# Performance work log

Hardware: AMD Instinct MI355X
Metric: run time of the kernel (lower is better)

## Reference

```python
import jax, jax.numpy as jnp
import numpy as np

HIDDEN = 4096
NH = 32        # num attention heads
NKV = 8        # num key/value heads
HD = 128       # q/k head dim
VHD = 96       # v head dim
ROT = 64       # rotary dim = int(HD * 0.5)
THETA = 10000.0
B, S = 2, 2048


def setup_inputs() -> dict:
    key = jax.random.key(0)
    ks = jax.random.split(key, 6)
    w = 0.02
    return {
        "hidden_states": jax.random.normal(ks[0], (B, S, HIDDEN), jnp.float32),
        "position_ids": jnp.arange(B * S, dtype=jnp.int32).reshape(B, S) % S,
        "Wq": jax.random.normal(ks[1], (NH * HD, HIDDEN), jnp.float32) * w,
        "Wk": jax.random.normal(ks[2], (NKV * HD, HIDDEN), jnp.float32) * w,
        "Wv": jax.random.normal(ks[3], (NKV * VHD, HIDDEN), jnp.float32) * w,
        "Wo": jax.random.normal(ks[4], (HIDDEN, NH * VHD), jnp.float32) * w,
    }


def _rotate_half(x):
    x1, x2 = x[..., : x.shape[-1] // 2], x[..., x.shape[-1] // 2 :]
    return jnp.concatenate((-x2, x1), axis=-1)


def reference(hidden_states, position_ids, Wq, Wk, Wv, Wo):
    b, s, _ = hidden_states.shape
    # QKV projections (torch Linear: y = x @ W^T)
    q = (hidden_states @ Wq.T).reshape(b, s, NH, HD).transpose(0, 2, 1, 3)   # [b,NH,s,HD]
    k = (hidden_states @ Wk.T).reshape(b, s, NKV, HD).transpose(0, 2, 1, 3)  # [b,NKV,s,HD]
    v = (hidden_states @ Wv.T).reshape(b, s, NKV, VHD).transpose(0, 2, 1, 3)  # [b,NKV,s,VHD]

    # rotary embedding over first ROT dims (partial RoPE)
    inv_freq = 1.0 / (THETA ** (jnp.arange(0, ROT, 2, dtype=jnp.float32) / ROT))  # [ROT/2]
    freqs = position_ids.astype(jnp.float32)[:, :, None] * inv_freq              # [b,s,ROT/2]
    emb = jnp.concatenate((freqs, freqs), axis=-1)                                # [b,s,ROT]
    cos = jnp.cos(emb)[:, None, :, :].astype(hidden_states.dtype)                 # [b,1,s,ROT]
    sin = jnp.sin(emb)[:, None, :, :].astype(hidden_states.dtype)

    q_rot, q_pass = q[..., :ROT], q[..., ROT:]
    k_rot, k_pass = k[..., :ROT], k[..., ROT:]
    q_rot = q_rot * cos + _rotate_half(q_rot) * sin
    k_rot = k_rot * cos + _rotate_half(k_rot) * sin
    q = jnp.concatenate((q_rot, q_pass), axis=-1)
    k = jnp.concatenate((k_rot, k_pass), axis=-1)

    # GQA: repeat_kv (repeat_interleave over head dim)
    n_rep = NH // NKV
    k = jnp.repeat(k, n_rep, axis=1)  # [b,NH,s,HD]
    v = jnp.repeat(v, n_rep, axis=1)  # [b,NH,s,VHD]

    scores = jnp.einsum("bhqd,bhkd->bhqk", q, k) / np.float32(np.sqrt(HD))
    # causal additive mask (attention_mask as built by the HF model)
    neg = jnp.finfo(jnp.float32).min
    causal = jnp.where(jnp.tril(jnp.ones((s, s), dtype=bool)), 0.0, neg)
    scores = scores + causal[None, None, :, :]

    attn = jax.nn.softmax(scores.astype(jnp.float32), axis=-1).astype(q.dtype)
    out = jnp.einsum("bhqk,bhkd->bhqd", attn, v)          # [b,NH,s,VHD]
    out = out.transpose(0, 2, 1, 3).reshape(b, s, NH * VHD)
    return out @ Wo.T                                      # [b,s,HIDDEN]
```

## Files before the change

kernel.cpp:

```cpp
#include <hip/hip_runtime.h>

typedef __attribute__((ext_vector_type(4))) float f32x4;
typedef __attribute__((ext_vector_type(8))) __bf16 bf16x8;
typedef __attribute__((ext_vector_type(8))) unsigned short u16x8;
typedef __attribute__((ext_vector_type(4))) unsigned short u16x4;
typedef __attribute__((ext_vector_type(4))) short s16x4;
typedef unsigned short ushort_t;

__device__ __forceinline__ unsigned short f2bf(float x) {
  unsigned u = __builtin_bit_cast(unsigned, x);
  u += 0x7fffu + ((u >> 16) & 1u);
  return (unsigned short)(u >> 16);
}
__device__ __forceinline__ float bf2f(unsigned short h) {
  unsigned u = ((unsigned)h) << 16;
  return __builtin_bit_cast(float, u);
}
__device__ __forceinline__ short f2bf_n(float x) {
  return __builtin_bit_cast(short, (__bf16)x);
}

__device__ __forceinline__ void gload_lds16(const void* g, void* l) {
  __builtin_amdgcn_global_load_lds(
      (const __attribute__((address_space(1))) unsigned int*)g,
      (__attribute__((address_space(3))) unsigned int*)l, 16, 0, 0);
}

__global__ __launch_bounds__(256) void k_f32_to_bf16(
    const float* __restrict__ src, ushort_t* __restrict__ dst, int n8) {
  int i = blockIdx.x * 256 + threadIdx.x;
  if (i >= n8) return;
  float4 a = ((const float4*)src)[i * 2 + 0];
  float4 b = ((const float4*)src)[i * 2 + 1];
  u16x8 o;
  o[0] = f2bf(a.x); o[1] = f2bf(a.y); o[2] = f2bf(a.z); o[3] = f2bf(a.w);
  o[4] = f2bf(b.x); o[5] = f2bf(b.y); o[6] = f2bf(b.z); o[7] = f2bf(b.w);
  ((u16x8*)dst)[i] = o;
}

template <int OUT_BF16, int ROPE>
__global__ __launch_bounds__(256, 4) void k_gemm_bt(
    const ushort_t* __restrict__ A, const ushort_t* __restrict__ B,
    void* __restrict__ C, int K, int lda, int ldb, int ldc,
    const int* __restrict__ pos_ids) {
  __shared__ ushort_t lA[128 * 64];
  __shared__ ushort_t lB[128 * 64];
  const int t = threadIdx.x;
  const int ln = t & 63, w = t >> 6;
  const int fr = ln & 15, fg = ln >> 4;
  const int m0 = blockIdx.x * 128, n0 = blockIdx.y * 128;
  const int wr = (w >> 1) * 64, wc = (w & 1) * 64;

  const int srow = t >> 3;
  const int scol = ((((t & 7) * 16) ^ ((srow & 7) << 4)) >> 1);
  const ushort_t* pA = A + (srow + m0) * lda + scol;
  const ushort_t* pB = B + (srow + n0) * ldb + scol;
  char* lAb = (char*)lA + (w << 10);
  char* lBb = (char*)lB + (w << 10);

  f32x4 acc[4][4] = {};

  for (int k0 = 0; k0 < K; k0 += 64) {
    __syncthreads();
#pragma unroll
    for (int i = 0; i < 4; ++i) {
      gload_lds16(pA + i * 32 * lda + k0, lAb + i * 4096);
      gload_lds16(pB + i * 32 * ldb + k0, lBb + i * 4096);
    }
    __syncthreads();
#pragma unroll
    for (int kh = 0; kh < 2; ++kh) {
      bf16x8 af[4], bfv[4];
#pragma unroll
      for (int m = 0; m < 4; ++m) {
        int row = wr + m * 16 + fr;
        af[m] = *(const bf16x8*)((const char*)lA + row * 128 +
                                 ((kh * 64 + fg * 16) ^ ((row & 7) << 4)));
      }
#pragma unroll
      for (int n = 0; n < 4; ++n) {
        int row = wc + n * 16 + fr;
        bfv[n] = *(const bf16x8*)((const char*)lB + row * 128 +
                                  ((kh * 64 + fg * 16) ^ ((row & 7) << 4)));
      }
#pragma unroll
      for (int m = 0; m < 4; ++m)
#pragma unroll
        for (int n = 0; n < 4; ++n)
          acc[m][n] = __builtin_amdgcn_mfma_f32_16x16x32_bf16(
              af[m], bfv[n], acc[m][n], 0, 0, 0);
    }
  }

  if (ROPE) {
    if (n0 < 5120 && wc == 0) {
#pragma unroll
      for (int n = 0; n < 2; ++n) {
        const float fi = (float)(n * 16 + fr);
        const float inv = exp2f(-fi * (13.287712379549449f / 32.0f));
#pragma unroll
        for (int m = 0; m < 4; ++m) {
          const int row = m0 + wr + m * 16 + fg * 4;
#pragma unroll
          for (int j = 0; j < 4; ++j) {
            const float ang = (float)pos_ids[row + j] * inv;
            float sn, cs;
            __sincosf(ang, &sn, &cs);
            const float x1 = acc[m][n][j], x2 = acc[m][n + 2][j];
            acc[m][n][j]     = x1 * cs - x2 * sn;
            acc[m][n + 2][j] = x2 * cs + x1 * sn;
          }
        }
      }
    }
  }

#pragma unroll
  for (int m = 0; m < 4; ++m)
#pragma unroll
    for (int n = 0; n < 4; ++n) {
      int row = m0 + wr + m * 16 + fg * 4;
      int col = n0 + wc + n * 16 + fr;
#pragma unroll
      for (int j = 0; j < 4; ++j) {
        if (OUT_BF16)
          ((ushort_t*)C)[(size_t)(row + j) * ldc + col] = f2bf(acc[m][n][j]);
        else
          ((float*)C)[(size_t)(row + j) * ldc + col] = acc[m][n][j];
      }
    }
}

__global__ __launch_bounds__(512, 2) void k_attn(
    const ushort_t* __restrict__ QKV, ushort_t* __restrict__ O) {
  __shared__ ushort_t lK[64 * 128];
  __shared__ ushort_t lV[16 * 96 * 4];

  const int t = threadIdx.x, ln = t & 63, w = t >> 6;
  const int fr = ln & 15, fg = ln >> 4;
  const int h = blockIdx.y, b = blockIdx.z;
  const int qt = b ? (7 - (int)blockIdx.x) : (int)blockIdx.x;
  const int hk = h >> 2;
  const int q0 = qt * 256 + w * 32;
  const int tb = b * 2048;

  bf16x8 qf[2][4];
#pragma unroll
  for (int rq = 0; rq < 2; ++rq)
#pragma unroll
    for (int kb = 0; kb < 4; ++kb)
      qf[rq][kb] = *(const bf16x8*)(QKV +
                    (size_t)(tb + q0 + rq * 16 + fr) * 5888 + h * 128 +
                    kb * 32 + fg * 8);

  f32x4 oacc[6][2] = {};
  float mreg[2] = {-1e30f, -1e30f};
  float lreg[2] = {0.f, 0.f};

  const int krow = t >> 4;
  const int kse = ((((t & 15) * 16) ^ (((t >> 4) & 7) << 4)) >> 1);
  const int k4s = t / 12, c8s = t % 12;

  const float sc = 0.088388347648318447f;
  const float l2e = 1.4426950408889634f;
  const float scl2e = sc * l2e;

  u16x8 vrow[4];
  const ushort_t* pVb =
      QKV + (size_t)(tb + k4s * 4) * 5888 + 5120 + hk * 96 + c8s * 8;
  if (t < 192) {
#pragma unroll
    for (int kr = 0; kr < 4; ++kr)
      vrow[kr] = *(const u16x8*)(pVb + (size_t)kr * 5888);
  }

  const int nkt = qt * 4 + 4;
  for (int kt = 0; kt < nkt; ++kt) {
    const int kb0 = kt * 64;
    __syncthreads();
    if (t < 192) {
#pragma unroll
      for (int i = 0; i < 8; ++i) {
        int cs = (c8s * 8 + i) ^ (k4s & 15);
        u16x4 q;
#pragma unroll
        for (int kr = 0; kr < 4; ++kr) q[kr] = vrow[kr][i];
        *(u16x4*)(&lV[(k4s * 96 + cs) * 4]) = q;
      }
    }
    {
      const ushort_t* pK =
          QKV + (size_t)(tb + kb0 + krow) * 5888 + 4096 + hk * 128 + kse;
#pragma unroll
      for (int i = 0; i < 2; ++i)
        gload_lds16(pK + (size_t)i * 32 * 5888,
                    (char*)lK + i * 8192 + (w << 10));
    }
    __builtin_amdgcn_sched_barrier(0);
    const bool pre = (kt + 1 < nkt);
    if (pre && t < 192) {
      const ushort_t* pV = pVb + (size_t)(kb0 + 64) * 5888;
#pragma unroll
      for (int kr = 0; kr < 4; ++kr)
        vrow[kr] = *(const u16x8*)(pV + (size_t)kr * 5888);
    }
    __builtin_amdgcn_sched_barrier(0);
    if (pre && w < 3)
      asm volatile("s_waitcnt vmcnt(4) lgkmcnt(0)" ::: "memory");
    else
      asm volatile("s_waitcnt vmcnt(0) lgkmcnt(0)" ::: "memory");
    __builtin_amdgcn_s_barrier();
    asm volatile("" ::: "memory");
    __builtin_amdgcn_sched_barrier(0);

    if (kb0 > q0 + 31) continue;
    f32x4 s[4][2] = {};
    __builtin_amdgcn_s_setprio(1);
#pragma unroll
    for (int cb = 0; cb < 4; ++cb) {
      const int kv = cb * 16 + fr;
      bf16x8 kf[4];
#pragma unroll
      for (int kb = 0; kb < 4; ++kb)
        kf[kb] = *(const bf16x8*)((const char*)lK + kv * 256 +
                                  ((kb * 64 + fg * 16) ^ ((kv & 7) << 4)));
#pragma unroll
      for (int rq = 0; rq < 2; ++rq)
#pragma unroll
        for (int kb = 0; kb < 4; ++kb)
          s[cb][rq] = __builtin_amdgcn_mfma_f32_16x16x32_bf16(
              kf[kb], qf[rq][kb], s[cb][rq], 0, 0, 0);
    }
    __builtin_amdgcn_s_setprio(0);
    if (kb0 + 63 > q0) {
#pragma unroll
      for (int rq = 0; rq < 2; ++rq) {
        const int qrel = q0 + rq * 16 + fr - kb0;
#pragma unroll
        for (int cb = 0; cb < 4; ++cb)
#pragma unroll
          for (int j = 0; j < 4; ++j)
            if (cb * 16 + fg * 4 + j > qrel) s[cb][rq][j] = -3.0e38f;
      }
    }
    float pmax[2];
#pragma unroll
    for (int rq = 0; rq < 2; ++rq) {
      f32x4 rm4 = s[0][rq];
#pragma unroll
      for (int cb = 1; cb < 4; ++cb)
#pragma unroll
        for (int j = 0; j < 4; ++j) rm4[j] = fmaxf(rm4[j], s[cb][rq][j]);
      float rm = fmaxf(fmaxf(rm4[0], rm4[1]), fmaxf(rm4[2], rm4[3]));
      rm = fmaxf(rm, __shfl_xor(rm, 16, 64));
      rm = fmaxf(rm, __shfl_xor(rm, 32, 64));
      pmax[rq] = rm * sc;
    }
    bool need = (pmax[0] > mreg[0] + 6.f) || (pmax[1] > mreg[1] + 6.f);
    if (__any(need)) {
#pragma unroll
      for (int rq = 0; rq < 2; ++rq) {
        float mnew = fmaxf(mreg[rq], pmax[rq]);
        float sf = exp2f((mreg[rq] - mnew) * l2e);
        mreg[rq] = mnew;
        lreg[rq] *= sf;
#pragma unroll
        for (int c6 = 0; c6 < 6; ++c6) oacc[c6][rq] *= sf;
      }
    }
    s16x4 pb[4][2];
#pragma unroll
    for (int rq = 0; rq < 2; ++rq) {
      const float mb = mreg[rq] * l2e;
      f32x4 ps4 = {};
#pragma unroll
      for (int cb = 0; cb < 4; ++cb) {
#pragma unroll
        for (int j = 0; j < 4; ++j) {
          float p = exp2f(fmaf(s[cb][rq][j], scl2e, -mb));
          s[cb][rq][j] = p;
          ps4[j] += p;
        }
      }
      float ps = (ps4[0] + ps4[1]) + (ps4[2] + ps4[3]);
      ps += __shfl_xor(ps, 16, 64);
      ps += __shfl_xor(ps, 32, 64);
      lreg[rq] += ps;
#pragma unroll
      for (int cb = 0; cb < 4; ++cb) {
        s16x4 v;
#pragma unroll
        for (int j = 0; j < 4; ++j) v[j] = f2bf_n(s[cb][rq][j]);
        pb[cb][rq] = v;
      }
    }
    __builtin_amdgcn_s_setprio(1);
#pragma unroll
    for (int cb = 0; cb < 4; ++cb) {
      const int k4 = cb * 4 + fg;
      s16x4 va[6];
#pragma unroll
      for (int c6 = 0; c6 < 6; ++c6)
        va[c6] = *(const s16x4*)(
            &lV[(k4 * 96 + (((c6 * 16 + fr) ^ (k4 & 15)))) * 4]);
#pragma unroll
      for (int c6 = 0; c6 < 6; ++c6)
#pragma unroll
        for (int rq = 0; rq < 2; ++rq)
          oacc[c6][rq] = __builtin_amdgcn_mfma_f32_16x16x16bf16_1k(
              va[c6], pb[cb][rq], oacc[c6][rq], 0, 0, 0);
    }
    __builtin_amdgcn_s_setprio(0);
  }
#pragma unroll
  for (int rq = 0; rq < 2; ++rq) {
    const float inv = 1.0f / lreg[rq];
    const size_t rowb = (size_t)(tb + q0 + rq * 16 + fr) * 3072 + h * 96;
#pragma unroll
    for (int c6 = 0; c6 < 6; ++c6) {
      u16x4 o;
#pragma unroll
      for (int j = 0; j < 4; ++j)
        o[j] = (unsigned short)f2bf_n(oacc[c6][rq][j] * inv);
      *(u16x4*)(&O[rowb + c6 * 16 + fg * 4]) = o;
    }
  }
}

extern "C" void kernel_launch(void* const* d_in, const int* in_sizes, int n_in,
                              void* d_out, int out_size, void* d_ws,
                              size_t ws_size, hipStream_t stream) {
  const float* X  = (const float*)d_in[0];
  const int*   pos = (const int*)d_in[1];
  const float* Wq = (const float*)d_in[2];
  const float* Wk = (const float*)d_in[3];
  const float* Wv = (const float*)d_in[4];
  const float* Wo = (const float*)d_in[5];
  float* out = (float*)d_out;

  ushort_t* Xb    = (ushort_t*)d_ws;
  ushort_t* Wob   = Xb + 16777216;
  ushort_t* QKV   = Wob + 12582912;
  ushort_t* AO    = QKV + 24117248;
  ushort_t* Wqkvb = (ushort_t*)d_out;

  k_f32_to_bf16<<<8192, 256, 0, stream>>>(X, Xb, 2097152);
  k_f32_to_bf16<<<8192, 256, 0, stream>>>(Wq, Wqkvb, 2097152);
  k_f32_to_bf16<<<2048, 256, 0, stream>>>(Wk, Wqkvb + 16777216, 524288);
  k_f32_to_bf16<<<1536, 256, 0, stream>>>(Wv, Wqkvb + 20971520, 393216);
  k_f32_to_bf16<<<6144, 256, 0, stream>>>(Wo, Wob, 1572864);

  k_gemm_bt<1, 1><<<dim3(32, 46), 256, 0, stream>>>(Xb, Wqkvb, QKV, 4096,
                                                    4096, 4096, 5888, pos);
  k_attn<<<dim3(8, 32, 2), 512, 0, stream>>>(QKV, AO);
  k_gemm_bt<0, 0><<<dim3(32, 32), 256, 0, stream>>>(AO, Wob, out, 3072, 3072,
                                                    3072, 4096, nullptr);
}
```

Before: 477.1 us.

## Double attention KV tile to 128 rows per barrier and fuse weight conversions

The attention kernel now stages 128 K/V rows per loop iteration instead of 64. Each staged tile is processed as two 64-row sub-blocks, so there are half as many block-wide barriers and global-to-LDS load phases per query tile. The cost is more LDS per block (about 56KB) and a coarser causal tail, where part of a staged tile may go unused. Separately, the four weight fp32-to-bf16 conversion launches are merged into one kernel that picks its source by block index, saving launch overhead.

Measured after the change: 455.6 us. 4.5% less time.

```diff
diff --git a/kernel.cpp b/kernel.cpp
--- a/kernel.cpp
+++ b/kernel.cpp
@@ -35,6 +35,27 @@
   u16x8 o;
   o[0] = f2bf(a.x); o[1] = f2bf(a.y); o[2] = f2bf(a.z); o[3] = f2bf(a.w);
   o[4] = f2bf(b.x); o[5] = f2bf(b.y); o[6] = f2bf(b.z); o[7] = f2bf(b.w);
+  ((u16x8*)dst)[i] = o;
+}
+
+__global__ __launch_bounds__(256) void k_w_to_bf16(
+    const float* __restrict__ Wq, const float* __restrict__ Wk,
+    const float* __restrict__ Wv, const float* __restrict__ Wo,
+    ushort_t* __restrict__ dWq, ushort_t* __restrict__ dWk,
+    ushort_t* __restrict__ dWv, ushort_t* __restrict__ dWo) {
+  const int b = blockIdx.x;
+  const float* src;
+  ushort_t* dst;
+  int i;
+  if (b < 8192)       { src = Wq; dst = dWq; i = b * 256 + threadIdx.x; }
+  else if (b < 10240) { src = Wk; dst = dWk; i = (b - 8192) * 256 + threadIdx.x; }
+  else if (b < 11776) { src = Wv; dst = dWv; i = (b - 10240) * 256 + threadIdx.x; }
+  else                { src = Wo; dst = dWo; i = (b - 11776) * 256 + threadIdx.x; }
+  float4 a = ((const float4*)src)[i * 2 + 0];
+  float4 c = ((const float4*)src)[i * 2 + 1];
+  u16x8 o;
+  o[0] = f2bf(a.x); o[1] = f2bf(a.y); o[2] = f2bf(a.z); o[3] = f2bf(a.w);
+  o[4] = f2bf(c.x); o[5] = f2bf(c.y); o[6] = f2bf(c.z); o[7] = f2bf(c.w);
   ((u16x8*)dst)[i] = o;
 }
 
@@ -133,8 +154,8 @@
 
 __global__ __launch_bounds__(512, 2) void k_attn(
     const ushort_t* __restrict__ QKV, ushort_t* __restrict__ O) {
-  __shared__ ushort_t lK[64 * 128];
-  __shared__ ushort_t lV[16 * 96 * 4];
+  __shared__ ushort_t lK[128 * 128];
+  __shared__ ushort_t lV[32 * 96 * 4];
 
   const int t = threadIdx.x, ln = t & 63, w = t >> 6;
   const int fr = ln & 15, fg = ln >> 4;
@@ -168,17 +189,17 @@
   u16x8 vrow[4];
   const ushort_t* pVb =
       QKV + (size_t)(tb + k4s * 4) * 5888 + 5120 + hk * 96 + c8s * 8;
-  if (t < 192) {
+  if (t < 384) {
 #pragma unroll
     for (int kr = 0; kr < 4; ++kr)
       vrow[kr] = *(const u16x8*)(pVb + (size_t)kr * 5888);
   }
 
-  const int nkt = qt * 4 + 4;
+  const int nkt = (qt + 1) * 2;
   for (int kt = 0; kt < nkt; ++kt) {
-    const int kb0 = kt * 64;
+    const int kb0t = kt * 128;
     __syncthreads();
-    if (t < 192) {
+    if (t < 384) {
 #pragma unroll
       for (int i = 0; i < 8; ++i) {
         int cs = (c8s * 8 + i) ^ (k4s & 15);
@@ -190,22 +211,22 @@
     }
     {
       const ushort_t* pK =
-          QKV + (size_t)(tb + kb0 + krow) * 5888 + 4096 + hk * 128 + kse;
-#pragma unroll
-      for (int i = 0; i < 2; ++i)
+          QKV + (size_t)(tb + kb0t + krow) * 5888 + 4096 + hk * 128 + kse;
+#pragma unroll
+      for (int i = 0; i < 4; ++i)
         gload_lds16(pK + (size_t)i * 32 * 5888,
                     (char*)lK + i * 8192 + (w << 10));
     }
     __builtin_amdgcn_sched_barrier(0);
     const bool pre = (kt + 1 < nkt);
-    if (pre && t < 192) {
-      const ushort_t* pV = pVb + (size_t)(kb0 + 64) * 5888;
+    if (pre && t < 384) {
+      const ushort_t* pV = pVb + (size_t)(kb0t + 128) * 5888;
 #pragma unroll
       for (int kr = 0; kr < 4; ++kr)
         vrow[kr] = *(const u16x8*)(pV + (size_t)kr * 5888);
     }
     __builtin_amdgcn_sched_barrier(0);
-    if (pre && w < 3)
+    if (pre && w < 6)
       asm volatile("s_waitcnt vmcnt(4) lgkmcnt(0)" ::: "memory");
     else
       asm volatile("s_waitcnt vmcnt(0) lgkmcnt(0)" ::: "memory");
@@ -213,104 +234,108 @@
     asm volatile("" ::: "memory");
     __builtin_amdgcn_sched_barrier(0);
 
-    if (kb0 > q0 + 31) continue;
-    f32x4 s[4][2] = {};
-    __builtin_amdgcn_s_setprio(1);
-#pragma unroll
-    for (int cb = 0; cb < 4; ++cb) {
-      const int kv = cb * 16 + fr;
-      bf16x8 kf[4];
-#pragma unroll
-      for (int kb = 0; kb < 4; ++kb)
-        kf[kb] = *(const bf16x8*)((const char*)lK + kv * 256 +
-                                  ((kb * 64 + fg * 16) ^ ((kv & 7) << 4)));
-#pragma unroll
-      for (int rq = 0; rq < 2; ++rq)
+#pragma unroll
+    for (int h64 = 0; h64 < 2; ++h64) {
+      const int kb0 = kb0t + h64 * 64;
+      if (kb0 > q0 + 31) break;
+      f32x4 s[4][2] = {};
+      __builtin_amdgcn_s_setprio(1);
+#pragma unroll
+      for (int cb = 0; cb < 4; ++cb) {
+        const int kv = h64 * 64 + cb * 16 + fr;
+        bf16x8 kf[4];
 #pragma unroll
         for (int kb = 0; kb < 4; ++kb)
-          s[cb][rq] = __builtin_amdgcn_mfma_f32_16x16x32_bf16(
-              kf[kb], qf[rq][kb], s[cb][rq], 0, 0, 0);
-    }
-    __builtin_amdgcn_s_setprio(0);
-    if (kb0 + 63 > q0) {
+          kf[kb] = *(const bf16x8*)((const char*)lK + kv * 256 +
+                                    ((kb * 64 + fg * 16) ^ ((kv & 7) << 4)));
+#pragma unroll
+        for (int rq = 0; rq < 2; ++rq)
+#pragma unroll
+          for (int kb = 0; kb < 4; ++kb)
+            s[cb][rq] = __builtin_amdgcn_mfma_f32_16x16x32_bf16(
+                kf[kb], qf[rq][kb], s[cb][rq], 0, 0, 0);
+      }
+      __builtin_amdgcn_s_setprio(0);
+      if (kb0 + 63 > q0) {
+#pragma unroll
+        for (int rq = 0; rq < 2; ++rq) {
+          const int qrel = q0 + rq * 16 + fr - kb0;
+#pragma unroll
+          for (int cb = 0; cb < 4; ++cb)
+#pragma unroll
+            for (int j = 0; j < 4; ++j)
+              if (cb * 16 + fg * 4 + j > qrel) s[cb][rq][j] = -3.0e38f;
+        }
+      }
+      float pmax[2];
 #pragma unroll
       for (int rq = 0; rq < 2; ++rq) {
-        const int qrel = q0 + rq * 16 + fr - kb0;
-#pragma unroll
-        for (int cb = 0; cb < 4; ++cb)
-#pragma unroll
-          for (int j = 0; j < 4; ++j)
-            if (cb * 16 + fg * 4 + j > qrel) s[cb][rq][j] = -3.0e38f;
-      }
-    }
-    float pmax[2];
-#pragma unroll
-    for (int rq = 0; rq < 2; ++rq) {
-      f32x4 rm4 = s[0][rq];
-#pragma unroll
-      for (int cb = 1; cb < 4; ++cb)
-#pragma unroll
-        for (int j = 0; j < 4; ++j) rm4[j] = fmaxf(rm4[j], s[cb][rq][j]);
-      float rm = fmaxf(fmaxf(rm4[0], rm4[1]), fmaxf(rm4[2], rm4[3]));
-      rm = fmaxf(rm, __shfl_xor(rm, 16, 64));
-      rm = fmaxf(rm, __shfl_xor(rm, 32, 64));
-      pmax[rq] = rm * sc;
-    }
-    bool need = (pmax[0] > mreg[0] + 6.f) || (pmax[1] > mreg[1] + 6.f);
-    if (__any(need)) {
+        f32x4 rm4 = s[0][rq];
+#pragma unroll
+        for (int cb = 1; cb < 4; ++cb)
+#pragma unroll
+          for (int j = 0; j < 4; ++j) rm4[j] = fmaxf(rm4[j], s[cb][rq][j]);
+        float rm = fmaxf(fmaxf(rm4[0], rm4[1]), fmaxf(rm4[2], rm4[3]));
+        rm = fmaxf(rm, __shfl_xor(rm, 16, 64));
+        rm = fmaxf(rm, __shfl_xor(rm, 32, 64));
+        pmax[rq] = rm * sc;
+      }
+      bool need = (pmax[0] > mreg[0] + 6.f) || (pmax[1] > mreg[1] + 6.f);
+      if (__any(need)) {
+#pragma unroll
+        for (int rq = 0; rq < 2; ++rq) {
+          float mnew = fmaxf(mreg[rq], pmax[rq]);
+          float sf = exp2f((mreg[rq] - mnew) * l2e);
+          mreg[rq] = mnew;
+          lreg[rq] *= sf;
+#pragma unroll
+          for (int c6 = 0; c6 < 6; ++c6) oacc[c6][rq] *= sf;
+        }
+      }
+      s16x4 pb[4][2];
 #pragma unroll
       for (int rq = 0; rq < 2; ++rq) {
-        float mnew = fmaxf(mreg[rq], pmax[rq]);
-        float sf = exp2f((mreg[rq] - mnew) * l2e);
-        mreg[rq] = mnew;
-        lreg[rq] *= sf;
-#pragma unroll
-        for (int c6 = 0; c6 < 6; ++c6) oacc[c6][rq] *= sf;
-      }
-    }
-    s16x4 pb[4][2];
-#pragma unroll
-    for (int rq = 0; rq < 2; ++rq) {
-      const float mb = mreg[rq] * l2e;
-      f32x4 ps4 = {};
+        const float mb = mreg[rq] * l2e;
+        f32x4 ps4 = {};
+#pragma unroll
+        for (int cb = 0; cb < 4; ++cb) {
+#pragma unroll
+          for (int j = 0; j < 4; ++j) {
+            float p = exp2f(fmaf(s[cb][rq][j], scl2e, -mb));
+            s[cb][rq][j] = p;
+            ps4[j] += p;
+          }
+        }
+        float ps = (ps4[0] + ps4[1]) + (ps4[2] + ps4[3]);
+        ps += __shfl_xor(ps, 16, 64);
+        ps += __shfl_xor(ps, 32, 64);
+        lreg[rq] += ps;
+#pragma unroll
+        for (int cb = 0; cb < 4; ++cb) {
+          s16x4 v;
+#pragma unroll
+          for (int j = 0; j < 4; ++j) v[j] = f2bf_n(s[cb][rq][j]);
+          pb[cb][rq] = v;
+        }
+      }
+      __builtin_amdgcn_s_setprio(1);
 #pragma unroll
       for (int cb = 0; cb < 4; ++cb) {
-#pragma unroll
-        for (int j = 0; j < 4; ++j) {
-          float p = exp2f(fmaf(s[cb][rq][j], scl2e, -mb));
-          s[cb][rq][j] = p;
-          ps4[j] += p;
-        }
-      }
-      float ps = (ps4[0] + ps4[1]) + (ps4[2] + ps4[3]);
-      ps += __shfl_xor(ps, 16, 64);
-      ps += __shfl_xor(ps, 32, 64);
-      lreg[rq] += ps;
-#pragma unroll
-      for (int cb = 0; cb < 4; ++cb) {
-        s16x4 v;
-#pragma unroll
-        for (int j = 0; j < 4; ++j) v[j] = f2bf_n(s[cb][rq][j]);
-        pb[cb][rq] = v;
-      }
-    }
-    __builtin_amdgcn_s_setprio(1);
-#pragma unroll
-    for (int cb = 0; cb < 4; ++cb) {
-      const int k4 = cb * 4 + fg;
-      s16x4 va[6];
-#pragma unroll
-      for (int c6 = 0; c6 < 6; ++c6)
-        va[c6] = *(const s16x4*)(
-            &lV[(k4 * 96 + (((c6 * 16 + fr) ^ (k4 & 15)))) * 4]);
-#pragma unroll
-      for (int c6 = 0; c6 < 6; ++c6)
-#pragma unroll
-        for (int rq = 0; rq < 2; ++rq)
-          oacc[c6][rq] = __builtin_amdgcn_mfma_f32_16x16x16bf16_1k(
-              va[c6], pb[cb][rq], oacc[c6][rq], 0, 0, 0);
-    }
-    __builtin_amdgcn_s_setprio(0);
+        const int k4 = h64 * 16 + cb * 4 + fg;
+        s16x4 va[6];
+#pragma unroll
+        for (int c6 = 0; c6 < 6; ++c6)
+          va[c6] = *(const s16x4*)(
+              &lV[(k4 * 96 + (((c6 * 16 + fr) ^ (k4 & 15)))) * 4]);
+#pragma unroll
+        for (int c6 = 0; c6 < 6; ++c6)
+#pragma unroll
+          for (int rq = 0; rq < 2; ++rq)
+            oacc[c6][rq] = __builtin_amdgcn_mfma_f32_16x16x16bf16_1k(
+                va[c6], pb[cb][rq], oacc[c6][rq], 0, 0, 0);
+      }
+      __builtin_amdgcn_s_setprio(0);
+    }
   }
 #pragma unroll
   for (int rq = 0; rq < 2; ++rq) {
@@ -345,10 +370,9 @@
   ushort_t* Wqkvb = (ushort_t*)d_out;
 
   k_f32_to_bf16<<<8192, 256, 0, stream>>>(X, Xb, 2097152);
-  k_f32_to_bf16<<<8192, 256, 0, stream>>>(Wq, Wqkvb, 2097152);
-  k_f32_to_bf16<<<2048, 256, 0, stream>>>(Wk, Wqkvb + 16777216, 524288);
-  k_f32_to_bf16<<<1536, 256, 0, stream>>>(Wv, Wqkvb + 20971520, 393216);
-  k_f32_to_bf16<<<6144, 256, 0, stream>>>(Wo, Wob, 1572864);
+  k_w_to_bf16<<<17920, 256, 0, stream>>>(Wq, Wk, Wv, Wo, Wqkvb,
+                                         Wqkvb + 16777216, Wqkvb + 20971520,
+                                         Wob);
 
   k_gemm_bt<1, 1><<<dim3(32, 46), 256, 0, stream>>>(Xb, Wqkvb, QKV, 4096,
                                                     4096, 4096, 5888, pos);
```
